# Kernel optimization log

Measured on AMD Instinct MI355X. Metric: run time of the kernel, lower is better.

The kernel has to match this reference:

```python
import jax, jax.numpy as jnp
import numpy as np
import math

FEAT_DIM = 128
N_BANK = 1000000
K_NEG = 4096
BATCH = 256
T = 0.5
MOMENTUM = 0.5
EPS = 1e-7


def setup_inputs() -> dict:
    key = jax.random.key(0)
    k1, k2, k3, k4, k5, k6 = jax.random.split(key, 6)
    stdv = 1.0 / math.sqrt(FEAT_DIM / 3)
    memory_l = jax.random.uniform(k1, (N_BANK, FEAT_DIM), minval=-stdv, maxval=stdv, dtype=jnp.float32)
    memory_ab = jax.random.uniform(k2, (N_BANK, FEAT_DIM), minval=-stdv, maxval=stdv, dtype=jnp.float32)
    l = jax.random.normal(k3, (BATCH, FEAT_DIM), dtype=jnp.float32)
    ab = jax.random.normal(k4, (BATCH, FEAT_DIM), dtype=jnp.float32)
    y = jax.random.randint(k5, (BATCH,), 0, N_BANK, dtype=jnp.int32)
    idx = jax.random.randint(k6, (BATCH, K_NEG + 1), 0, N_BANK, dtype=jnp.int32)
    idx = idx.at[:, 0].set(y)  # positive sample in slot 0, as in torch forward
    return {"l": l, "ab": ab, "memory_l": memory_l, "memory_ab": memory_ab, "y": y, "idx": idx}


def _l2_normalize(x):
    # matches torch: x / (sqrt(sum(x^2)) + eps)
    return x / (jnp.sqrt(jnp.sum(x * x, axis=1, keepdims=True)) + EPS)


def _momentum_update(memory, y, x_norm):
    # gather rows, momentum mix, renormalize, scatter back
    pos = memory[y] * MOMENTUM + x_norm * (1.0 - MOMENTUM)          # [B, D]
    norm = jnp.sqrt(jnp.sum(pos * pos, axis=1, keepdims=True))
    return memory.at[y].set(pos / norm)


def reference(l, ab, memory_l, memory_ab, y, idx):
    outputSize = memory_l.shape[0]
    ln = _l2_normalize(l)
    abn = _l2_normalize(ab)

    # gather negatives+positive from the AB bank, score against l features
    w_ab = jax.lax.stop_gradient(memory_ab[idx])                     # [B, K+1, D]
    P_l = jnp.exp(jnp.einsum('bkd,bd->bk', w_ab, ln) / T)[..., None]  # [B, K+1, 1]
    Z_l = jnp.mean(P_l) * outputSize
    out_l = P_l / Z_l

    w_l = jax.lax.stop_gradient(memory_l[idx])                       # [B, K+1, D]
    P_ab = jnp.exp(jnp.einsum('bkd,bd->bk', w_l, abn) / T)[..., None]
    Z_ab = jnp.mean(P_ab) * outputSize
    out_ab = P_ab / Z_ab

    # momentum scatter update of the memory banks (no_grad in torch)
    new_memory_l = jax.lax.stop_gradient(_momentum_update(memory_l, y, ln))
    new_memory_ab = jax.lax.stop_gradient(_momentum_update(memory_ab, y, abn))

    return out_l, out_ab, new_memory_l, new_memory_ab
```

## Files before the change

kernel.cpp:

```cpp
#include <hip/hip_runtime.h>
#include <math.h>

#define FEAT   128
#define NBANK  1000000
#define KP1    4097
#define BATCH  256
#define INV_T  2.0f
#define EPS_N  1e-7f

constexpr size_t TOTP   = (size_t)BATCH * KP1;
constexpr size_t O_OUTL = 0;
constexpr size_t O_OUTA = TOTP;
constexpr size_t O_MEML = 2 * TOTP;
constexpr size_t O_MEMA = O_MEML + (size_t)NBANK * FEAT;

constexpr int KCHUNK = 64;
constexpr int NCHUNK = (KP1 + KCHUNK - 1) / KCHUNK;
constexpr int NPART  = BATCH * NCHUNK;
constexpr int SCOREB = BATCH * NCHUNK;

constexpr size_t N4      = (size_t)NBANK * FEAT / 4;
constexpr size_t CSTRIDE = (size_t)SCOREB * 256;

constexpr size_t WS_LN    = 0;
constexpr size_t WS_ABN   = WS_LN + (size_t)BATCH * FEAT;
constexpr size_t WS_PARTL = WS_ABN + (size_t)BATCH * FEAT;
constexpr size_t WS_PARTA = WS_PARTL + NPART;
constexpr size_t WS_INVZ  = WS_PARTA + NPART;

typedef float vfloat4 __attribute__((ext_vector_type(4)));

__device__ __forceinline__ void nt_store4(vfloat4* p, vfloat4 v) {
    __builtin_nontemporal_store(v, p);
}
__device__ __forceinline__ float dot4(vfloat4 a, vfloat4 b) {
    return a.x * b.x + a.y * b.y + a.z * b.z + a.w * b.w;
}

__global__ void norm_kernel(const float* __restrict__ l,
                            const float* __restrict__ ab,
                            float* __restrict__ ws) {
    int b    = blockIdx.x;
    int lane = threadIdx.x;
    const float* src;
    float*       dst;
    if (b < BATCH) { src = l  + (size_t)b * FEAT;            dst = ws + WS_LN  + (size_t)b * FEAT; }
    else           { src = ab + (size_t)(b - BATCH) * FEAT;  dst = ws + WS_ABN + (size_t)(b - BATCH) * FEAT; }
    float2 v = *(const float2*)(src + 2 * lane);
    float  ss = v.x * v.x + v.y * v.y;
    #pragma unroll
    for (int m = 1; m < 64; m <<= 1) ss += __shfl_xor(ss, m, 64);
    float inv = 1.0f / (sqrtf(ss) + EPS_N);
    ((float2*)dst)[lane] = make_float2(v.x * inv, v.y * inv);
}

__global__ __launch_bounds__(256) void fused_kernel(
        const float* __restrict__ mem_l, const float* __restrict__ mem_ab,
        const int*   __restrict__ idx,
        const float* __restrict__ ws_in,
        float* __restrict__ out,
        float* __restrict__ part_l, float* __restrict__ part_ab) {
    int sid    = blockIdx.x;
    int b      = sid % BATCH;
    int chunk  = sid / BATCH;
    int wave   = threadIdx.x >> 6;
    int lane   = threadIdx.x & 63;
    int lane16 = lane & 15;
    int g      = lane >> 4;

    const vfloat4* lnp = (const vfloat4*)(ws_in + WS_LN  + (size_t)b * FEAT);
    const vfloat4* abp = (const vfloat4*)(ws_in + WS_ABN + (size_t)b * FEAT);
    vfloat4 lv0 = lnp[lane16 * 2], lv1 = lnp[lane16 * 2 + 1];
    vfloat4 av0 = abp[lane16 * 2], av1 = abp[lane16 * 2 + 1];

    const vfloat4* ca = (const vfloat4*)mem_l;
    const vfloat4* cb = (const vfloat4*)mem_ab;
    vfloat4* ol = (vfloat4*)(out + O_MEML);
    vfloat4* oa = (vfloat4*)(out + O_MEMA);
    size_t cbase = (size_t)sid * 256 + threadIdx.x;

    const int* idx_b = idx + (size_t)b * KP1;
    int kw = chunk * KCHUNK + wave * 16;

    float sum_l = 0.f, sum_ab = 0.f;
    #pragma unroll
    for (int t = 0; t < 4; ++t) {
        #pragma unroll
        for (int j = 0; j < 2; ++j) {
            size_t ci = cbase + (size_t)(2 * t + j) * CSTRIDE;
            if (ci < N4) {
                nt_store4(ol + ci, ca[ci]);
                nt_store4(oa + ci, cb[ci]);
            }
        }
        int k = kw + t * 4 + g;
        bool valid = k < KP1;
        int row = valid ? idx_b[k] : 0;
        const vfloat4* pa = (const vfloat4*)(mem_ab + (size_t)row * FEAT) + lane16 * 2;
        const vfloat4* pw = (const vfloat4*)(mem_l  + (size_t)row * FEAT) + lane16 * 2;
        vfloat4 wa0 = pa[0], wa1 = pa[1];
        vfloat4 wl0 = pw[0], wl1 = pw[1];
        float dl  = dot4(wa0, lv0) + dot4(wa1, lv1);
        float dab = dot4(wl0, av0) + dot4(wl1, av1);
        #pragma unroll
        for (int m = 1; m < 16; m <<= 1) {
            dl  += __shfl_xor(dl,  m, 64);
            dab += __shfl_xor(dab, m, 64);
        }
        float pl  = valid ? __expf(dl  * INV_T) : 0.f;
        float pab = valid ? __expf(dab * INV_T) : 0.f;
        if (lane16 == 0 && valid) {
            out[O_OUTL + (size_t)b * KP1 + k] = pl;
            out[O_OUTA + (size_t)b * KP1 + k] = pab;
        }
        sum_l += pl; sum_ab += pab;
    }
    #pragma unroll
    for (int m = 16; m < 64; m <<= 1) {
        sum_l  += __shfl_xor(sum_l,  m, 64);
        sum_ab += __shfl_xor(sum_ab, m, 64);
    }
    __shared__ float s[8];
    if (lane == 0) { s[wave] = sum_l; s[4 + wave] = sum_ab; }
    __syncthreads();
    if (threadIdx.x == 0) {
        part_l[(size_t)b * NCHUNK + chunk]  = s[0] + s[1] + s[2] + s[3];
        part_ab[(size_t)b * NCHUNK + chunk] = s[4] + s[5] + s[6] + s[7];
    }
}

__global__ void zreduce_kernel(const float* __restrict__ part_l,
                               const float* __restrict__ part_ab,
                               float* __restrict__ invz) {
    __shared__ float sl[256], sa[256];
    float a = 0.f, b = 0.f;
    for (int i = threadIdx.x; i < NPART; i += 256) { a += part_l[i]; b += part_ab[i]; }
    sl[threadIdx.x] = a; sa[threadIdx.x] = b;
    __syncthreads();
    for (int s = 128; s > 0; s >>= 1) {
        if (threadIdx.x < (unsigned)s) {
            sl[threadIdx.x] += sl[threadIdx.x + s];
            sa[threadIdx.x] += sa[threadIdx.x + s];
        }
        __syncthreads();
    }
    if (threadIdx.x == 0) {
        float count = (float)TOTP;
        invz[0] = count / (sl[0] * (float)NBANK);
        invz[1] = count / (sa[0] * (float)NBANK);
    }
}

__global__ void scale_kernel(float* __restrict__ out, const float* __restrict__ invz) {
    float zl = invz[0], za = invz[1];
    size_t stride = (size_t)gridDim.x * blockDim.x;
    for (size_t i = (size_t)blockIdx.x * blockDim.x + threadIdx.x; i < TOTP; i += stride) {
        out[O_OUTL + i] *= zl;
        out[O_OUTA + i] *= za;
    }
}

__global__ void update_kernel(const float* __restrict__ mem_l,
                              const float* __restrict__ mem_ab,
                              const int*   __restrict__ y,
                              const float* __restrict__ ws,
                              float* __restrict__ out) {
    int b    = blockIdx.x;
    int lane = threadIdx.x;
    int row  = y[b];
    for (int j = b + 1; j < BATCH; ++j)
        if (y[j] == row) return;
    {
        float2 m = ((const float2*)(mem_l + (size_t)row * FEAT))[lane];
        float2 x = ((const float2*)(ws + WS_LN + (size_t)b * FEAT))[lane];
        float2 p = make_float2(m.x * 0.5f + x.x * 0.5f, m.y * 0.5f + x.y * 0.5f);
        float ss = p.x * p.x + p.y * p.y;
        #pragma unroll
        for (int mk = 1; mk < 64; mk <<= 1) ss += __shfl_xor(ss, mk, 64);
        float nrm = sqrtf(ss);
        ((float2*)(out + O_MEML + (size_t)row * FEAT))[lane] =
            make_float2(p.x / nrm, p.y / nrm);
    }
    {
        float2 m = ((const float2*)(mem_ab + (size_t)row * FEAT))[lane];
        float2 x = ((const float2*)(ws + WS_ABN + (size_t)b * FEAT))[lane];
        float2 p = make_float2(m.x * 0.5f + x.x * 0.5f, m.y * 0.5f + x.y * 0.5f);
        float ss = p.x * p.x + p.y * p.y;
        #pragma unroll
        for (int mk = 1; mk < 64; mk <<= 1) ss += __shfl_xor(ss, mk, 64);
        float nrm = sqrtf(ss);
        ((float2*)(out + O_MEMA + (size_t)row * FEAT))[lane] =
            make_float2(p.x / nrm, p.y / nrm);
    }
}

extern "C" void kernel_launch(void* const* d_in, const int* in_sizes, int n_in,
                              void* d_out, int out_size, void* d_ws, size_t ws_size,
                              hipStream_t stream) {
    const float* l      = (const float*)d_in[0];
    const float* ab     = (const float*)d_in[1];
    const float* mem_l  = (const float*)d_in[2];
    const float* mem_ab = (const float*)d_in[3];
    const int*   y      = (const int*)d_in[4];
    const int*   idx    = (const int*)d_in[5];
    float* out = (float*)d_out;
    float* ws  = (float*)d_ws;

    norm_kernel<<<dim3(2 * BATCH), dim3(64), 0, stream>>>(l, ab, ws);
    fused_kernel<<<dim3(SCOREB), dim3(256), 0, stream>>>(
        mem_l, mem_ab, idx, ws, out, ws + WS_PARTL, ws + WS_PARTA);
    zreduce_kernel<<<dim3(1), dim3(256), 0, stream>>>(ws + WS_PARTL, ws + WS_PARTA, ws + WS_INVZ);
    scale_kernel<<<dim3(1024), dim3(256), 0, stream>>>(out, ws + WS_INVZ);
    update_kernel<<<dim3(BATCH), dim3(64), 0, stream>>>(mem_l, mem_ab, y, ws, out);
}
```

Measured before the change: 583.2 us.

## Bucket gather indices by bank row and score from LDS-staged bank tiles

Replaces the random per-(batch,k) gather from both memory banks with a counting sort of all indices into 32-row buckets (histogram, scan, scatter). Each block then streams its 32 bank rows once, copies them to the output banks and to LDS, and scores every index that points into those rows using LDS reads. The bank-copy traffic now doubles as the gather traffic, removing roughly a second pass of random global reads. In exchange it adds atomics-heavy sort kernels, a single-block serial scan over 31250 buckets, random-order output writes and a separate Z-sum pass.

```diff
diff --git a/kernel.cpp b/kernel.cpp
--- a/kernel.cpp
+++ b/kernel.cpp
@@ -1,5 +1,6 @@
 #include <hip/hip_runtime.h>
 #include <math.h>
+#include <stdint.h>
 
 #define FEAT   128
 #define NBANK  1000000
@@ -14,19 +15,15 @@
 constexpr size_t O_MEML = 2 * TOTP;
 constexpr size_t O_MEMA = O_MEML + (size_t)NBANK * FEAT;
 
-constexpr int KCHUNK = 64;
-constexpr int NCHUNK = (KP1 + KCHUNK - 1) / KCHUNK;
-constexpr int NPART  = BATCH * NCHUNK;
-constexpr int SCOREB = BATCH * NCHUNK;
-
-constexpr size_t N4      = (size_t)NBANK * FEAT / 4;
-constexpr size_t CSTRIDE = (size_t)SCOREB * 256;
-
-constexpr size_t WS_LN    = 0;
-constexpr size_t WS_ABN   = WS_LN + (size_t)BATCH * FEAT;
-constexpr size_t WS_PARTL = WS_ABN + (size_t)BATCH * FEAT;
-constexpr size_t WS_PARTA = WS_PARTL + NPART;
-constexpr size_t WS_INVZ  = WS_PARTA + NPART;
+constexpr int RPB   = 32;
+constexpr int NBUCK = NBANK / RPB;
+
+constexpr size_t WS_LN   = 0;
+constexpr size_t WS_ABN  = 32768;
+constexpr size_t WS_INVZ = 65536;
+constexpr size_t WS_PL   = 65544;
+constexpr size_t WS_PA   = 65800;
+constexpr size_t WS_U32  = 66560;
 
 typedef float vfloat4 __attribute__((ext_vector_type(4)));
 
@@ -54,52 +51,105 @@
     ((float2*)dst)[lane] = make_float2(v.x * inv, v.y * inv);
 }
 
-__global__ __launch_bounds__(256) void fused_kernel(
+__global__ void zero_kernel(unsigned int* __restrict__ cnt) {
+    int stride = gridDim.x * blockDim.x;
+    for (int i = blockIdx.x * blockDim.x + threadIdx.x; i < NBUCK; i += stride)
+        cnt[i] = 0u;
+}
+
+__global__ void hist_kernel(const int* __restrict__ idx,
+                            unsigned int* __restrict__ cnt) {
+    int stride = gridDim.x * blockDim.x;
+    for (size_t p = (size_t)blockIdx.x * blockDim.x + threadIdx.x; p < TOTP; p += stride) {
+        int row = idx[p];
+        atomicAdd(&cnt[row >> 5], 1u);
+    }
+}
+
+__global__ void scan_kernel(const unsigned int* __restrict__ cnt,
+                            unsigned int* __restrict__ start,
+                            unsigned int* __restrict__ cur) {
+    __shared__ unsigned int ts[256];
+    __shared__ unsigned int ex[256];
+    int t = threadIdx.x;
+    const int Q = (NBUCK + 255) / 256;
+    int lo = t * Q, hi = lo + Q; if (hi > NBUCK) hi = NBUCK;
+    unsigned int s = 0;
+    for (int i = lo; i < hi; ++i) s += cnt[i];
+    ts[t] = s;
+    __syncthreads();
+    if (t == 0) {
+        unsigned int r = 0;
+        for (int i = 0; i < 256; ++i) { ex[i] = r; r += ts[i]; }
+    }
+    __syncthreads();
+    unsigned int base = ex[t];
+    for (int i = lo; i < hi; ++i) {
+        start[i] = base; cur[i] = base;
+        base += cnt[i];
+    }
+}
+
+__global__ void scatter_kernel(const int* __restrict__ idx,
+                               unsigned int* __restrict__ cur,
+                               unsigned int* __restrict__ ent) {
+    int stride = gridDim.x * blockDim.x;
+    for (size_t p = (size_t)blockIdx.x * blockDim.x + threadIdx.x; p < TOTP; p += stride) {
+        int row = idx[p];
+        int b   = (int)(p / KP1);
+        int k   = (int)(p - (size_t)b * KP1);
+        unsigned int pos = atomicAdd(&cur[row >> 5], 1u);
+        ent[pos] = ((unsigned int)b << 18) | ((unsigned int)k << 5) | (unsigned int)(row & 31);
+    }
+}
+
+__global__ __launch_bounds__(256) void main_kernel(
         const float* __restrict__ mem_l, const float* __restrict__ mem_ab,
-        const int*   __restrict__ idx,
-        const float* __restrict__ ws_in,
-        float* __restrict__ out,
-        float* __restrict__ part_l, float* __restrict__ part_ab) {
-    int sid    = blockIdx.x;
-    int b      = sid % BATCH;
-    int chunk  = sid / BATCH;
-    int wave   = threadIdx.x >> 6;
-    int lane   = threadIdx.x & 63;
-    int lane16 = lane & 15;
-    int g      = lane >> 4;
-
-    const vfloat4* lnp = (const vfloat4*)(ws_in + WS_LN  + (size_t)b * FEAT);
-    const vfloat4* abp = (const vfloat4*)(ws_in + WS_ABN + (size_t)b * FEAT);
-    vfloat4 lv0 = lnp[lane16 * 2], lv1 = lnp[lane16 * 2 + 1];
-    vfloat4 av0 = abp[lane16 * 2], av1 = abp[lane16 * 2 + 1];
-
-    const vfloat4* ca = (const vfloat4*)mem_l;
-    const vfloat4* cb = (const vfloat4*)mem_ab;
-    vfloat4* ol = (vfloat4*)(out + O_MEML);
-    vfloat4* oa = (vfloat4*)(out + O_MEMA);
-    size_t cbase = (size_t)sid * 256 + threadIdx.x;
-
-    const int* idx_b = idx + (size_t)b * KP1;
-    int kw = chunk * KCHUNK + wave * 16;
-
-    float sum_l = 0.f, sum_ab = 0.f;
-    #pragma unroll
-    for (int t = 0; t < 4; ++t) {
-        #pragma unroll
-        for (int j = 0; j < 2; ++j) {
-            size_t ci = cbase + (size_t)(2 * t + j) * CSTRIDE;
-            if (ci < N4) {
-                nt_store4(ol + ci, ca[ci]);
-                nt_store4(oa + ci, cb[ci]);
-            }
-        }
-        int k = kw + t * 4 + g;
-        bool valid = k < KP1;
-        int row = valid ? idx_b[k] : 0;
-        const vfloat4* pa = (const vfloat4*)(mem_ab + (size_t)row * FEAT) + lane16 * 2;
-        const vfloat4* pw = (const vfloat4*)(mem_l  + (size_t)row * FEAT) + lane16 * 2;
-        vfloat4 wa0 = pa[0], wa1 = pa[1];
-        vfloat4 wl0 = pw[0], wl1 = pw[1];
+        const float* __restrict__ ws_f,
+        const unsigned int* __restrict__ start,
+        const unsigned int* __restrict__ cur,
+        const unsigned int* __restrict__ ent,
+        float* __restrict__ out) {
+    __shared__ float ldsL[RPB * FEAT];
+    __shared__ float ldsA[RPB * FEAT];
+    int blk = blockIdx.x;
+    int tid = threadIdx.x;
+    size_t fbase = (size_t)blk * RPB * FEAT;
+
+    const vfloat4* sl = (const vfloat4*)(mem_l  + fbase);
+    const vfloat4* sa = (const vfloat4*)(mem_ab + fbase);
+    vfloat4* dl_ = (vfloat4*)(out + O_MEML + fbase);
+    vfloat4* da_ = (vfloat4*)(out + O_MEMA + fbase);
+    vfloat4* lL = (vfloat4*)ldsL;
+    vfloat4* lA = (vfloat4*)ldsA;
+    vfloat4 vl[4], va[4];
+    #pragma unroll
+    for (int j = 0; j < 4; ++j) { vl[j] = sl[j * 256 + tid]; }
+    #pragma unroll
+    for (int j = 0; j < 4; ++j) { va[j] = sa[j * 256 + tid]; }
+    #pragma unroll
+    for (int j = 0; j < 4; ++j) {
+        int i = j * 256 + tid;
+        lL[i] = vl[j]; nt_store4(dl_ + i, vl[j]);
+        lA[i] = va[j]; nt_store4(da_ + i, va[j]);
+    }
+    __syncthreads();
+
+    int s = (int)start[blk], e = (int)cur[blk];
+    int g = tid >> 4, lane16 = tid & 15;
+    for (int i = s + g; i < e; i += 16) {
+        unsigned int ev = ent[i];
+        int rloc = (int)(ev & 31u);
+        int k    = (int)((ev >> 5) & 0x1FFFu);
+        int b    = (int)(ev >> 18);
+        const vfloat4* ra = (const vfloat4*)(ldsA + rloc * FEAT) + lane16 * 2;
+        const vfloat4* rl = (const vfloat4*)(ldsL + rloc * FEAT) + lane16 * 2;
+        vfloat4 wa0 = ra[0], wa1 = ra[1];
+        vfloat4 wl0 = rl[0], wl1 = rl[1];
+        const vfloat4* lq = (const vfloat4*)(ws_f + WS_LN  + (size_t)b * FEAT) + lane16 * 2;
+        const vfloat4* aq = (const vfloat4*)(ws_f + WS_ABN + (size_t)b * FEAT) + lane16 * 2;
+        vfloat4 lv0 = lq[0], lv1 = lq[1];
+        vfloat4 av0 = aq[0], av1 = aq[1];
         float dl  = dot4(wa0, lv0) + dot4(wa1, lv1);
         float dab = dot4(wl0, av0) + dot4(wl1, av1);
         #pragma unroll
@@ -107,47 +157,39 @@
             dl  += __shfl_xor(dl,  m, 64);
             dab += __shfl_xor(dab, m, 64);
         }
-        float pl  = valid ? __expf(dl  * INV_T) : 0.f;
-        float pab = valid ? __expf(dab * INV_T) : 0.f;
-        if (lane16 == 0 && valid) {
-            out[O_OUTL + (size_t)b * KP1 + k] = pl;
-            out[O_OUTA + (size_t)b * KP1 + k] = pab;
+        if (lane16 == 0) {
+            out[O_OUTL + (size_t)b * KP1 + k] = __expf(dl  * INV_T);
+            out[O_OUTA + (size_t)b * KP1 + k] = __expf(dab * INV_T);
         }
-        sum_l += pl; sum_ab += pab;
-    }
-    #pragma unroll
-    for (int m = 16; m < 64; m <<= 1) {
-        sum_l  += __shfl_xor(sum_l,  m, 64);
-        sum_ab += __shfl_xor(sum_ab, m, 64);
-    }
-    __shared__ float s[8];
-    if (lane == 0) { s[wave] = sum_l; s[4 + wave] = sum_ab; }
-    __syncthreads();
+    }
+}
+
+__global__ void zsum_kernel(const float* __restrict__ out,
+                            float* __restrict__ pl, float* __restrict__ pa) {
+    __shared__ float sl[256], sa[256];
+    int i = blockIdx.x, t = threadIdx.x;
+    const float* bl = out + O_OUTL + (size_t)i * KP1;
+    const float* ba = out + O_OUTA + (size_t)i * KP1;
+    float a = 0.f, b = 0.f;
+    for (int p = t; p < KP1; p += 256) { a += bl[p]; b += ba[p]; }
+    sl[t] = a; sa[t] = b;
+    __syncthreads();
+    for (int s = 128; s > 0; s >>= 1) {
+        if (t < s) { sl[t] += sl[t + s]; sa[t] += sa[t + s]; }
+        __syncthreads();
+    }
+    if (t == 0) { pl[i] = sl[0]; pa[i] = sa[0]; }
+}
+
+__global__ void zfinal_kernel(const float* __restrict__ pl,
+                              const float* __restrict__ pa,
+                              float* __restrict__ invz) {
     if (threadIdx.x == 0) {
-        part_l[(size_t)b * NCHUNK + chunk]  = s[0] + s[1] + s[2] + s[3];
-        part_ab[(size_t)b * NCHUNK + chunk] = s[4] + s[5] + s[6] + s[7];
-    }
-}
-
-__global__ void zreduce_kernel(const float* __restrict__ part_l,
-                               const float* __restrict__ part_ab,
-                               float* __restrict__ invz) {
-    __shared__ float sl[256], sa[256];
-    float a = 0.f, b = 0.f;
-    for (int i = threadIdx.x; i < NPART; i += 256) { a += part_l[i]; b += part_ab[i]; }
-    sl[threadIdx.x] = a; sa[threadIdx.x] = b;
-    __syncthreads();
-    for (int s = 128; s > 0; s >>= 1) {
-        if (threadIdx.x < (unsigned)s) {
-            sl[threadIdx.x] += sl[threadIdx.x + s];
-            sa[threadIdx.x] += sa[threadIdx.x + s];
-        }
-        __syncthreads();
-    }
-    if (threadIdx.x == 0) {
+        float a = 0.f, b = 0.f;
+        for (int i = 0; i < 256; ++i) { a += pl[i]; b += pa[i]; }
         float count = (float)TOTP;
-        invz[0] = count / (sl[0] * (float)NBANK);
-        invz[1] = count / (sa[0] * (float)NBANK);
+        invz[0] = count / (a * (float)NBANK);
+        invz[1] = count / (b * (float)NBANK);
     }
 }
 
@@ -206,10 +248,21 @@
     float* out = (float*)d_out;
     float* ws  = (float*)d_ws;
 
+    unsigned int* wsu   = (unsigned int*)(ws + WS_U32);
+    unsigned int* cnt   = wsu;
+    unsigned int* start = wsu + NBUCK;
+    unsigned int* cur   = wsu + 2 * (size_t)NBUCK;
+    unsigned int* ent   = wsu + 3 * (size_t)NBUCK;
+
     norm_kernel<<<dim3(2 * BATCH), dim3(64), 0, stream>>>(l, ab, ws);
-    fused_kernel<<<dim3(SCOREB), dim3(256), 0, stream>>>(
-        mem_l, mem_ab, idx, ws, out, ws + WS_PARTL, ws + WS_PARTA);
-    zreduce_kernel<<<dim3(1), dim3(256), 0, stream>>>(ws + WS_PARTL, ws + WS_PARTA, ws + WS_INVZ);
+    zero_kernel   <<<dim3(128),  dim3(256), 0, stream>>>(cnt);
+    hist_kernel   <<<dim3(2048), dim3(256), 0, stream>>>(idx, cnt);
+    scan_kernel   <<<dim3(1),    dim3(256), 0, stream>>>(cnt, start, cur);
+    scatter_kernel<<<dim3(2048), dim3(256), 0, stream>>>(idx, cur, ent);
+    main_kernel<<<dim3(NBUCK), dim3(256), 0, stream>>>(
+        mem_l, mem_ab, ws, start, cur, ent, out);
+    zsum_kernel  <<<dim3(256), dim3(256), 0, stream>>>(out, ws + WS_PL, ws + WS_PA);
+    zfinal_kernel<<<dim3(1),   dim3(64),  0, stream>>>(ws + WS_PL, ws + WS_PA, ws + WS_INVZ);
     scale_kernel<<<dim3(1024), dim3(256), 0, stream>>>(out, ws + WS_INVZ);
     update_kernel<<<dim3(BATCH), dim3(64), 0, stream>>>(mem_l, mem_ab, y, ws, out);
 }
```

Result: no change. 577.5 us (-1.0%).
